# Kernel tuning notes

Measured on AMD Instinct MI355X. Metric: run time of the kernel, lower is better.

The kernel has to match this reference:

```python
import jax, jax.numpy as jnp
import numpy as np

B, L, D_IN = 16, 2048, 512
HID, H = 512, 8
D = HID // H          # head dim
FACTOR = 5
U = min(FACTOR * int(np.ceil(np.log(L))), L)  # u_q == u_k == 40 (L == S)


def setup_inputs() -> dict:
    key = jax.random.key(0)
    ks = jax.random.split(key, 8)
    s = 1.0 / np.sqrt(D_IN).astype(np.float32)
    return {
        "q_in": jax.random.normal(ks[0], (B, L, D_IN), jnp.float32),
        "k_in": jax.random.normal(ks[1], (B, L, D_IN), jnp.float32),
        "v_in": jax.random.normal(ks[2], (B, L, D_IN), jnp.float32),
        "Wq": jax.random.normal(ks[3], (D_IN, HID), jnp.float32) * s,
        "Wk": jax.random.normal(ks[4], (D_IN, HID), jnp.float32) * s,
        "Wv": jax.random.normal(ks[5], (D_IN, HID), jnp.float32) * s,
        "Wo": jax.random.normal(ks[6], (HID, HID // H), jnp.float32) / np.sqrt(HID).astype(np.float32),
        "indx_q_seq": jax.random.randint(ks[7], (L,), 0, L, dtype=jnp.int32),
    }


def reference(q_in, k_in, v_in, Wq, Wk, Wv, Wo, indx_q_seq):
    # projections + (memory-reinterpreting, as in the TF source) head reshape
    q = (q_in @ Wq).reshape(B, H, L, D)
    k = (k_in @ Wk).reshape(B, H, L, D)
    v = (v_in @ Wv).reshape(B, H, L, D)

    # --- _prob_qk ---
    # TF's chained gathers on the broadcast k_expand collapse to pairing
    # query s with the single key indx_q_seq[s]; all sample_k columns of
    # Q_K_sample are identical, so M = max - sum/L = dot * (1 - U/L).
    k_sel = k[:, :, indx_q_seq, :]                        # [B,H,L,D]
    dot = jnp.einsum('bhle,bhle->bhl', q, k_sel)          # [B,H,L]
    M = dot - dot * (jnp.float32(U) / jnp.float32(L))
    _, m_top = jax.lax.top_k(M, U)                        # [B,H,U]

    b_idx = jnp.arange(B)[:, None, None]
    h_idx = jnp.arange(H)[None, :, None]
    q_red = q[b_idx, h_idx, m_top]                        # [B,H,U,D]
    scores = jnp.einsum('bhue,bhle->bhul', q_red, k)      # [B,H,U,L]
    scores = scores * (1.0 / np.sqrt(D).astype(np.float32))

    # --- initial context: causal cumsum of values ---
    context = jnp.cumsum(v, axis=-2)                      # [B,H,L,D]

    # --- update context at the top-U query positions (causal mask) ---
    causal = jnp.arange(L)[None, None, None, :] > m_top[..., None]
    scores = jnp.where(causal, -jnp.inf, scores)
    attn = jax.nn.softmax(scores, axis=-1)                # [B,H,U,L]
    upd = jnp.einsum('bhul,bhld->bhud', attn, v)          # [B,H,U,D]
    context = context.at[b_idx, h_idx, m_top].set(upd)

    out = context.reshape(B, L, HID) @ Wo                 # [B,L,HID//H]
    return out
```

## Files before the change

kernel.cpp:

```cpp
#include <hip/hip_runtime.h>
#include <hip/hip_bf16.h>
#include <math.h>

#define B_   16
#define L_   2048
#define DIN  512
#define HID_ 512
#define H_   8
#define D_   64
#define U_   40
#define BH   (B_*H_)

typedef unsigned short u16;
typedef unsigned int u32;
typedef unsigned long long u64;
typedef __bf16 bf16x8 __attribute__((ext_vector_type(8)));
typedef float f32x4 __attribute__((ext_vector_type(4)));

__device__ __forceinline__ u16 f2bf(float x) {
  __bf16 b = (__bf16)x;
  return __builtin_bit_cast(unsigned short, b);
}
__device__ __forceinline__ float bf2f(u16 h) {
  return __uint_as_float(((unsigned)h) << 16);
}
__device__ __forceinline__ float bflo(u32 x) { return __uint_as_float(x << 16); }
__device__ __forceinline__ float bfhi(u32 x) { return __uint_as_float(x & 0xFFFF0000u); }
__device__ __forceinline__ u32 pk2(float a, float b) {
  return (u32)f2bf(a) | ((u32)f2bf(b) << 16);
}
__device__ __forceinline__ void gload16(const u16* g, u16* l) {
  __builtin_amdgcn_global_load_lds(
      (__attribute__((address_space(1))) void*)(g),
      (__attribute__((address_space(3))) void*)(l), 16, 0, 0);
}
__device__ __forceinline__ void gload16f(const float* g, float* l) {
  __builtin_amdgcn_global_load_lds(
      (__attribute__((address_space(1))) void*)(g),
      (__attribute__((address_space(3))) void*)(l), 16, 0, 0);
}
__device__ __forceinline__ u64 mkkey(float Mv, int l) {
  u32 fb = __float_as_uint(Mv);
  u32 mapped = (fb & 0x80000000u) ? ~fb : (fb | 0x80000000u);
  return ((u64)mapped << 32) | (u64)(0xFFFFFFFFu - (u32)l);
}

__global__ __launch_bounds__(256)
void wsplit3_kernel(const float* __restrict__ Wq, const float* __restrict__ Wk,
                    const float* __restrict__ Wv, u16* __restrict__ Bt3) {
  const float* W = (blockIdx.y == 0) ? Wq : (blockIdx.y == 1) ? Wk : Wv;
  u16* Bt = Bt3 + (size_t)blockIdx.y * 524288;
  int tid = blockIdx.x * 256 + threadIdx.x;
  int n = tid & 511, k = tid >> 9;
  float a = W[(size_t)k * 512 + n];
  u16 hi = f2bf(a);
  u16 lo = f2bf(a - bf2f(hi));
  int kb = k >> 5, kc = k & 31;
  int slotH = kc >> 3, wi = kc & 7;
  int swzH = (slotH     ^ (n & 7)) << 3;
  int swzL = ((4+slotH) ^ (n & 7)) << 3;
  Bt[(size_t)n * 1024 + kb * 64 + swzH + wi] = hi;
  Bt[(size_t)n * 1024 + kb * 64 + swzL + wi] = lo;
}

template<int NPASS, int OUTBF>
__global__ __launch_bounds__(256, 4)
void gemm_proj(const float* __restrict__ A, const u16* __restrict__ Bt,
               void* __restrict__ C) {
  __shared__ float Asf[128 * 32];
  __shared__ u16 Bs[128 * 64];
  const int bid = blockIdx.x;
  const int g = bid >> 3;
  const int xb = (bid & 7) + ((g >> 2) << 3);
  const int yb = g & 3;
  const int t = threadIdx.x;
  const int w = t >> 6, lane = t & 63;
  const int lhi = lane >> 4, l16 = lane & 15;
  const int row0 = xb * 128, col0 = yb * 128;
  const int wrow = (w >> 1) * 64, wcol = (w & 1) * 64;

  const u16* gB = Bt + (size_t)(col0 + w * 32 + (lane >> 3)) * 1024 + (lane & 7) * 8;
  u16* lB = &Bs[(w * 32) * 64];

  const int rA0 = w * 32 + (lane >> 3);
  const int swsl = lane & 7;

  f32x4 acc[4][4];
  #pragma unroll
  for (int i = 0; i < 4; ++i)
    #pragma unroll
    for (int j = 0; j < 4; ++j) acc[i][j] = (f32x4){0.f, 0.f, 0.f, 0.f};

  for (int kb = 0; kb < 16; ++kb) {
    #pragma unroll
    for (int i = 0; i < 4; ++i)
      gload16(gB + kb * 64 + (size_t)i * 8 * 1024, lB + i * 8 * 64);
    #pragma unroll
    for (int i = 0; i < 4; ++i) {
      int r = rA0 + i * 8;
      int slot = swsl ^ (r & 7);
      gload16f(A + (size_t)(row0 + r) * 512 + kb * 32 + slot * 4,
               &Asf[(w * 32 + i * 8) * 32]);
    }
    __syncthreads();

    bf16x8 bfH[4], bfL[4];
    #pragma unroll
    for (int j = 0; j < 4; ++j) {
      int cb = wcol + j * 16 + l16;
      bfH[j] = *reinterpret_cast<const bf16x8*>(
          &Bs[cb * 64 + ((lhi ^ (cb & 7)) << 3)]);
      if constexpr (NPASS == 3)
        bfL[j] = *reinterpret_cast<const bf16x8*>(
            &Bs[cb * 64 + (((4 + lhi) ^ (cb & 7)) << 3)]);
    }
    #pragma unroll
    for (int i = 0; i < 4; ++i) {
      int ra = wrow + i * 16 + l16;
      const f32x4 x0 = *reinterpret_cast<const f32x4*>(
          &Asf[ra * 32 + (((lhi * 2)       ^ (ra & 7)) << 2)]);
      const f32x4 x1 = *reinterpret_cast<const f32x4*>(
          &Asf[ra * 32 + ((((lhi * 2) + 1) ^ (ra & 7)) << 2)]);
      bf16x8 aH;
      aH[0] = (__bf16)x0[0]; aH[1] = (__bf16)x0[1];
      aH[2] = (__bf16)x0[2]; aH[3] = (__bf16)x0[3];
      aH[4] = (__bf16)x1[0]; aH[5] = (__bf16)x1[1];
      aH[6] = (__bf16)x1[2]; aH[7] = (__bf16)x1[3];
      #pragma unroll
      for (int j = 0; j < 4; ++j)
        acc[i][j] = __builtin_amdgcn_mfma_f32_16x16x32_bf16(aH, bfH[j], acc[i][j], 0, 0, 0);
      if constexpr (NPASS == 3) {
        bf16x8 aL;
        aL[0] = (__bf16)(x0[0] - (float)aH[0]); aL[1] = (__bf16)(x0[1] - (float)aH[1]);
        aL[2] = (__bf16)(x0[2] - (float)aH[2]); aL[3] = (__bf16)(x0[3] - (float)aH[3]);
        aL[4] = (__bf16)(x1[0] - (float)aH[4]); aL[5] = (__bf16)(x1[1] - (float)aH[5]);
        aL[6] = (__bf16)(x1[2] - (float)aH[6]); aL[7] = (__bf16)(x1[3] - (float)aH[7]);
        #pragma unroll
        for (int j = 0; j < 4; ++j)
          acc[i][j] = __builtin_amdgcn_mfma_f32_16x16x32_bf16(aH, bfL[j], acc[i][j], 0, 0, 0);
        #pragma unroll
        for (int j = 0; j < 4; ++j)
          acc[i][j] = __builtin_amdgcn_mfma_f32_16x16x32_bf16(aL, bfH[j], acc[i][j], 0, 0, 0);
      }
    }
    __syncthreads();
  }
  #pragma unroll
  for (int i = 0; i < 4; ++i)
    #pragma unroll
    for (int j = 0; j < 4; ++j)
      #pragma unroll
      for (int r = 0; r < 4; ++r) {
        size_t idx = (size_t)(row0 + wrow + i * 16 + lhi * 4 + r) * 512
                     + col0 + wcol + j * 16 + l16;
        if constexpr (OUTBF) ((u16*)C)[idx] = f2bf(acc[i][j][r]);
        else                 ((float*)C)[idx] = acc[i][j][r];
      }
}

__global__ __launch_bounds__(256)
void dotsel_kernel(const float* __restrict__ qp, const float* __restrict__ kp,
                   const int* __restrict__ indx, u64* __restrict__ cand) {
  __shared__ u64 keys[256];
  __shared__ u64 wmax[2][4];
  const int bh = blockIdx.x, ch = blockIdx.y;
  const int t = threadIdx.x, w = t >> 6, lane = t & 63;
  const size_t boff = (size_t)bh * 131072;
  const int l0 = ch * 256 + w * 64;
  const float cUL = 40.0f / 2048.0f;
  const int li = lane >> 4;
  const int dq = lane & 15;

  #pragma unroll 4
  for (int i = 0; i < 16; ++i) {
    int l = l0 + i * 4 + li;
    int ls = indx[l];
    float4 q4 = *reinterpret_cast<const float4*>(&qp[boff + (size_t)l * 64 + dq * 4]);
    float4 k4 = *reinterpret_cast<const float4*>(&kp[boff + (size_t)ls * 64 + dq * 4]);
    float p = q4.x * k4.x + q4.y * k4.y + q4.z * k4.z + q4.w * k4.w;
    p += __shfl_xor(p, 1, 64);
    p += __shfl_xor(p, 2, 64);
    p += __shfl_xor(p, 4, 64);
    p += __shfl_xor(p, 8, 64);
    if (dq == 0) {
      float Mv = p - p * cUL;
      keys[w * 64 + i * 4 + li] = mkkey(Mv, l);
    }
  }
  __syncthreads();

  u64 myk = keys[t];
  for (int u = 0; u < U_; ++u) {
    u64 b = myk;
    #pragma unroll
    for (int off = 32; off >= 1; off >>= 1) {
      u64 v = __shfl_xor(b, off, 64);
      if (v > b) b = v;
    }
    if (lane == 0) wmax[u & 1][w] = b;
    __syncthreads();
    const u64* wm = wmax[u & 1];
    u64 m = wm[0];
    if (wm[1] > m) m = wm[1];
    if (wm[2] > m) m = wm[2];
    if (wm[3] > m) m = wm[3];
    if (myk == m) myk = 0;
    if (t == 0) cand[((size_t)(bh * 8 + ch)) * U_ + u] = m;
  }
}

__global__ __launch_bounds__(64)
void merge_topk(const u64* __restrict__ cand, int* __restrict__ mtop) {
  const int bh = blockIdx.x;
  const int lane = threadIdx.x;
  u64 c0 = cand[(size_t)bh * 320 + 0 * 64 + lane];
  u64 c1 = cand[(size_t)bh * 320 + 1 * 64 + lane];
  u64 c2 = cand[(size_t)bh * 320 + 2 * 64 + lane];
  u64 c3 = cand[(size_t)bh * 320 + 3 * 64 + lane];
  u64 c4 = cand[(size_t)bh * 320 + 4 * 64 + lane];
  for (int u = 0; u < U_; ++u) {
    u64 b = c0;
    if (c1 > b) b = c1;
    if (c2 > b) b = c2;
    if (c3 > b) b = c3;
    if (c4 > b) b = c4;
    #pragma unroll
    for (int off = 32; off >= 1; off >>= 1) {
      u64 v = __shfl_xor(b, off, 64);
      if (v > b) b = v;
    }
    if (c0 == b) c0 = 0;
    if (c1 == b) c1 = 0;
    if (c2 == b) c2 = 0;
    if (c3 == b) c3 = 0;
    if (c4 == b) c4 = 0;
    if (lane == 0) mtop[bh * U_ + u] = (int)(0xFFFFFFFFu - (u32)b);
  }
}

__global__ __launch_bounds__(256)
void gather_q_kernel(const float* __restrict__ qp, const int* __restrict__ mtop,
                     u16* __restrict__ qredbf) {
  int tid = blockIdx.x * 256 + threadIdx.x;
  int s = tid >> 6;
  int d = tid & 63;
  int bh = s / 48;
  int u = s - bh * 48;
  float val = 0.f;
  if (u < U_) {
    int m = mtop[bh * U_ + u];
    val = qp[(size_t)bh * (L_ * D_) + (size_t)m * D_ + d] * 0.125f;
  }
  qredbf[tid] = f2bf(val);
}

__global__ __launch_bounds__(256)
void scores_mfma(const u16* __restrict__ qredbf, const float* __restrict__ kp,
                 const int* __restrict__ mtop, u16* __restrict__ S) {
  __shared__ u16 As[48 * 64];
  __shared__ u16 Bs[128 * 64];
  __shared__ int ms[U_];
  const int bh = blockIdx.x;
  const int l0 = blockIdx.y * 128;
  const int t = threadIdx.x, w = t >> 6, lane = t & 63;
  const int lhi = lane >> 4, l16 = lane & 15;

  for (int e = t; e < 384; e += 256) {
    int r = e >> 3, s = e & 7;
    *reinterpret_cast<uint4*>(&As[r * 64 + ((s ^ (r & 7)) << 3)]) =
        *reinterpret_cast<const uint4*>(&qredbf[(size_t)bh * 3072 + e * 8]);
  }
  #pragma unroll
  for (int ee = 0; ee < 4; ++ee) {
    int e = t + ee * 256;
    int r = e >> 3, s = e & 7;
    const float* src = &kp[(size_t)bh * 131072 + (size_t)(l0 + r) * 64 + s * 8];
    float4 va = *reinterpret_cast<const float4*>(src);
    float4 vb = *reinterpret_cast<const float4*>(src + 4);
    uint4 w4 = make_uint4(pk2(va.x, va.y), pk2(va.z, va.w),
                          pk2(vb.x, vb.y), pk2(vb.z, vb.w));
    *reinterpret_cast<uint4*>(&Bs[r * 64 + ((s ^ (r & 7)) << 3)]) = w4;
  }
  if (t < U_) ms[t] = mtop[bh * U_ + t];
  __syncthreads();

  f32x4 acc[3][2];
  #pragma unroll
  for (int m = 0; m < 3; ++m)
    #pragma unroll
    for (int n = 0; n < 2; ++n) acc[m][n] = (f32x4){0.f, 0.f, 0.f, 0.f};

  #pragma unroll
  for (int ks = 0; ks < 2; ++ks) {
    bf16x8 a[3], b[2];
    #pragma unroll
    for (int m = 0; m < 3; ++m) {
      int r = m * 16 + l16;
      a[m] = *reinterpret_cast<const bf16x8*>(
          &As[r * 64 + (((ks * 4 + lhi) ^ (r & 7)) << 3)]);
    }
    #pragma unroll
    for (int n = 0; n < 2; ++n) {
      int cb = w * 32 + n * 16 + l16;
      b[n] = *reinterpret_cast<const bf16x8*>(
          &Bs[cb * 64 + (((ks * 4 + lhi) ^ (cb & 7)) << 3)]);
    }
    #pragma unroll
    for (int m = 0; m < 3; ++m)
      #pragma unroll
      for (int n = 0; n < 2; ++n)
        acc[m][n] = __builtin_amdgcn_mfma_f32_16x16x32_bf16(a[m], b[n], acc[m][n], 0, 0, 0);
  }

  #pragma unroll
  for (int m = 0; m < 3; ++m)
    #pragma unroll
    for (int n = 0; n < 2; ++n)
      #pragma unroll
      for (int r = 0; r < 4; ++r) {
        int u = m * 16 + lhi * 4 + r;
        if (u < U_) {
          int l = l0 + w * 32 + n * 16 + l16;
          float val = acc[m][n][r];
          if (l > ms[u]) val = -INFINITY;
          S[((size_t)bh * 48 + u) * 2048 + l] = f2bf(val);
        }
      }
}

__global__ __launch_bounds__(256)
void softmax_kernel(u16* __restrict__ S) {
  __shared__ float red[4];
  const int rr = blockIdx.x;
  const int bh = rr / U_;
  const int u = rr - bh * U_;
  const int t = threadIdx.x;
  uint4* rp = reinterpret_cast<uint4*>(&S[((size_t)bh * 48 + u) * 2048]);
  uint4 raw = rp[t];
  float f[8];
  f[0] = bflo(raw.x); f[1] = bfhi(raw.x); f[2] = bflo(raw.y); f[3] = bfhi(raw.y);
  f[4] = bflo(raw.z); f[5] = bfhi(raw.z); f[6] = bflo(raw.w); f[7] = bfhi(raw.w);
  float m = f[0];
  #pragma unroll
  for (int i = 1; i < 8; ++i) m = fmaxf(m, f[i]);
  #pragma unroll
  for (int off = 32; off >= 1; off >>= 1) m = fmaxf(m, __shfl_xor(m, off, 64));
  if ((t & 63) == 0) red[t >> 6] = m;
  __syncthreads();
  m = fmaxf(fmaxf(red[0], red[1]), fmaxf(red[2], red[3]));
  __syncthreads();
  float s = 0.f;
  #pragma unroll
  for (int i = 0; i < 8; ++i) { f[i] = expf(f[i] - m); s += f[i]; }
  #pragma unroll
  for (int off = 32; off >= 1; off >>= 1) s += __shfl_xor(s, off, 64);
  if ((t & 63) == 0) red[t >> 6] = s;
  __syncthreads();
  s = red[0] + red[1] + red[2] + red[3];
  float inv = 1.0f / s;
  uint4 o;
  o.x = pk2(f[0] * inv, f[1] * inv);
  o.y = pk2(f[2] * inv, f[3] * inv);
  o.z = pk2(f[4] * inv, f[5] * inv);
  o.w = pk2(f[6] * inv, f[7] * inv);
  rp[t] = o;
}

__global__ __launch_bounds__(256)
void pv_mfma(const u16* __restrict__ Pbf, const u16* __restrict__ vbf,
             float* __restrict__ partial) {
  __shared__ u16 Ps[48 * 128];
  __shared__ u16 Vs[64 * 128];
  const int bh = blockIdx.x, kh = blockIdx.y;
  const int t = threadIdx.x, w = t >> 6, lane = t & 63;
  const int lhi = lane >> 4, l16 = lane & 15;
  const size_t vbase = (size_t)bh * 131072;
  f32x4 acc[3];
  #pragma unroll
  for (int m = 0; m < 3; ++m) acc[m] = (f32x4){0.f, 0.f, 0.f, 0.f};

  for (int ch = 0; ch < 2; ++ch) {
    const int lb = kh * 256 + ch * 128;
    for (int e = t; e < 768; e += 256) {
      int r = e >> 4, s = e & 15;
      int sw = (s & 8) | ((s & 7) ^ (r & 7));
      *reinterpret_cast<uint4*>(&Ps[r * 128 + (sw << 3)]) =
          *reinterpret_cast<const uint4*>(&Pbf[((size_t)bh * 48 + r) * 2048 + lb + s * 8]);
    }
    #pragma unroll
    for (int j = 0; j < 16; ++j) {
      int ll = w * 32 + 2 * j;
      u16 ua = vbf[vbase + (size_t)(lb + ll) * 64 + lane];
      u16 ub = vbf[vbase + (size_t)(lb + ll + 1) * 64 + lane];
      u32 pk = (u32)ua | ((u32)ub << 16);
      int s = ll >> 3;
      int sw = (s & 8) | ((s & 7) ^ (lane & 7));
      *reinterpret_cast<u32*>(&Vs[lane * 128 + (sw << 3) + (ll & 7)]) = pk;
    }
    __syncthreads();
    #pragma unroll
    for (int ks = 0; ks < 4; ++ks) {
      bf16x8 b;
      { int cb = w * 16 + l16; int s = ks * 4 + lhi;
        int sw = (s & 8) | ((s & 7) ^ (cb & 7));
        b = *reinterpret_cast<const bf16x8*>(&Vs[cb * 128 + (sw << 3)]); }
      #pragma unroll
      for (int m = 0; m < 3; ++m) {
        int r = m * 16 + l16; int s = ks * 4 + lhi;
        int sw = (s & 8) | ((s & 7) ^ (r & 7));
        bf16x8 a = *reinterpret_cast<const bf16x8*>(&Ps[r * 128 + (sw << 3)]);
        acc[m] = __builtin_amdgcn_mfma_f32_16x16x32_bf16(a, b, acc[m], 0, 0, 0);
      }
    }
    __syncthreads();
  }
  #pragma unroll
  for (int m = 0; m < 3; ++m)
    #pragma unroll
    for (int r = 0; r < 4; ++r) {
      int u = m * 16 + lhi * 4 + r;
      partial[(((size_t)kh * 128 + bh) * 48 + u) * 64 + w * 16 + l16] = acc[m][r];
    }
}

__global__ __launch_bounds__(256)
void cumsumA(const u16* __restrict__ vbf, float* __restrict__ seg32) {
  int bh = blockIdx.x, sg = blockIdx.y;
  int t = threadIdx.x, w = t >> 6, lane = t & 63;
  int g = sg * 4 + w;
  size_t base = (size_t)bh * 131072 + (size_t)g * 32 * 64;
  float s = 0.f;
  for (int i = 0; i < 32; ++i) s += bf2f(vbf[base + i * 64 + lane]);
  seg32[((size_t)bh * 64 + g) * 64 + lane] = s;
}
__global__ __launch_bounds__(256)
void cumsumB(const u16* __restrict__ vbf, const float* __restrict__ seg32,
             float* __restrict__ ctx) {
  int bh = blockIdx.x, sg = blockIdx.y;
  int t = threadIdx.x, w = t >> 6, lane = t & 63;
  int g = sg * 4 + w;
  float run = 0.f;
  for (int s = 0; s < g; ++s) run += seg32[((size_t)bh * 64 + s) * 64 + lane];
  size_t base = (size_t)bh * 131072 + (size_t)g * 32 * 64;
  for (int i = 0; i < 32; ++i) {
    run += bf2f(vbf[base + i * 64 + lane]);
    ctx[base + i * 64 + lane] = run;
  }
}

__global__ __launch_bounds__(256)
void scatter_kernel(const float* __restrict__ partial, const int* __restrict__ mtop,
                    float* __restrict__ ctx) {
  int tid = blockIdx.x * 256 + threadIdx.x;
  int s = tid >> 6;
  if (s >= BH * U_) return;
  int d = tid & 63;
  int bh = s / U_;
  int u = s - bh * U_;
  float a = 0.f;
  #pragma unroll
  for (int c = 0; c < 8; ++c)
    a += partial[(((size_t)(c * 128 + bh)) * 48 + u) * 64 + d];
  ctx[(size_t)bh * 131072 + (size_t)mtop[s] * 64 + d] = a;
}

__global__ __launch_bounds__(256)
void wo_prep(const float* __restrict__ Wo, u16* __restrict__ WoT) {
  int tid = blockIdx.x * 256 + threadIdx.x;
  int j = tid >> 9, k = tid & 511;
  float v = Wo[(size_t)k * 64 + j];
  int k0 = k & ~63, ko = k & 63;
  int ks = ko >> 5, kc = ko & 31;
  int slot = (ks * 4 + (kc >> 3)) ^ (j & 7);
  WoT[(size_t)j * 512 + k0 + (slot << 3) + (kc & 7)] = f2bf(v);
}

__global__ __launch_bounds__(256, 6)
void gemm_out(const float* __restrict__ ctx, const u16* __restrict__ WoT,
              float* __restrict__ out) {
  __shared__ u16 As[64 * 64];
  __shared__ u16 Bs[64 * 64];
  const int t = threadIdx.x, w = t >> 6, lane = t & 63;
  const int lhi = lane >> 4, l16 = lane & 15;
  const int row0 = blockIdx.x * 64;
  f32x4 acc[4];
  #pragma unroll
  for (int j = 0; j < 4; ++j) acc[j] = (f32x4){0.f, 0.f, 0.f, 0.f};

  for (int k0 = 0; k0 < 512; k0 += 64) {
    #pragma unroll
    for (int ii = 0; ii < 2; ++ii) {
      int e = t + ii * 256;
      int j = e >> 3, s = e & 7;
      gload16(WoT + (size_t)j * 512 + k0 + s * 8, Bs + (size_t)(w * 64 + ii * 256) * 8);
    }
    #pragma unroll
    for (int ii = 0; ii < 2; ++ii) {
      int e = t + ii * 256;
      int r = e >> 3, s = e & 7;
      const float* src = &ctx[(size_t)(row0 + r) * 512 + k0 + s * 8];
      float4 va = *reinterpret_cast<const float4*>(src);
      float4 vb = *reinterpret_cast<const float4*>(src + 4);
      uint4 w4 = make_uint4(pk2(va.x, va.y), pk2(va.z, va.w),
                            pk2(vb.x, vb.y), pk2(vb.z, vb.w));
      *reinterpret_cast<uint4*>(&As[r * 64 + ((s ^ (r & 7)) << 3)]) = w4;
    }
    __syncthreads();
    #pragma unroll
    for (int ks = 0; ks < 2; ++ks) {
      int r = w * 16 + l16;
      bf16x8 a = *reinterpret_cast<const bf16x8*>(
          &As[r * 64 + (((ks * 4 + lhi) ^ (r & 7)) << 3)]);
      #pragma unroll
      for (int jf = 0; jf < 4; ++jf) {
        int cb = jf * 16 + l16;
        bf16x8 b = *reinterpret_cast<const bf16x8*>(
            &Bs[cb * 64 + (((ks * 4 + lhi) ^ (cb & 7)) << 3)]);
        acc[jf] = __builtin_amdgcn_mfma_f32_16x16x32_bf16(a, b, acc[jf], 0, 0, 0);
      }
    }
    __syncthreads();
  }
  #pragma unroll
  for (int jf = 0; jf < 4; ++jf)
    #pragma unroll
    for (int r = 0; r < 4; ++r)
      out[(size_t)(row0 + w * 16 + lhi * 4 + r) * 64 + jf * 16 + l16] = acc[jf][r];
}

extern "C" void kernel_launch(void* const* d_in, const int* in_sizes, int n_in,
                              void* d_out, int out_size, void* d_ws, size_t ws_size,
                              hipStream_t stream) {
  const float* q_in = (const float*)d_in[0];
  const float* k_in = (const float*)d_in[1];
  const float* v_in = (const float*)d_in[2];
  const float* Wq   = (const float*)d_in[3];
  const float* Wk   = (const float*)d_in[4];
  const float* Wv   = (const float*)d_in[5];
  const float* Wo   = (const float*)d_in[6];
  const int*   indx = (const int*)d_in[7];
  float* out = (float*)d_out;

  float* ws = (float*)d_ws;
  float* qp   = ws;
  float* kp   = ws + 16777216;
  u16*   vbf  = (u16*)(ws + 33554432);
  u64*   cand = (u64*)(ws + 50331648);
  u16*   WoT  = (u16*)cand;
  u16*   qredbf = (u16*)(ws + 50593792);
  int*   mtop = (int*)(ws + 50921472);
  u16*   Bt3  = (u16*)d_out;
  u16*   S    = (u16*)qp;
  float* ctx  = qp;
  float* partial = kp;
  float* seg32   = kp + 3145728;

  const int M = B_ * L_;

  wsplit3_kernel<<<dim3(1024, 3), 256, 0, stream>>>(Wq, Wk, Wv, Bt3);

  gemm_proj<3, 0><<<1024, 256, 0, stream>>>(q_in, Bt3, qp);
  gemm_proj<3, 0><<<1024, 256, 0, stream>>>(k_in, Bt3 + 524288, kp);
  gemm_proj<1, 1><<<1024, 256, 0, stream>>>(v_in, Bt3 + 1048576, vbf);

  dotsel_kernel<<<dim3(BH, 8), 256, 0, stream>>>(qp, kp, indx, cand);
  merge_topk<<<BH, 64, 0, stream>>>(cand, mtop);
  gather_q_kernel<<<(BH * 48 * 64) / 256, 256, 0, stream>>>(qp, mtop, qredbf);

  scores_mfma<<<dim3(BH, 16), 256, 0, stream>>>(qredbf, kp, mtop, S);
  softmax_kernel<<<BH * U_, 256, 0, stream>>>(S);
  pv_mfma<<<dim3(BH, 8), 256, 0, stream>>>(S, vbf, partial);

  cumsumA<<<dim3(BH, 16), 256, 0, stream>>>(vbf, seg32);
  cumsumB<<<dim3(BH, 16), 256, 0, stream>>>(vbf, seg32, ctx);

  scatter_kernel<<<(BH * U_ * 64) / 256, 256, 0, stream>>>(partial, mtop, ctx);

  wo_prep<<<128, 256, 0, stream>>>(Wo, WoT);
  gemm_out<<<M / 64, 256, 0, stream>>>(ctx, WoT, out);
}
```

Measured before the change: 341.0 us.

## Fuse scores, softmax and PV into split-softmax kernel; bf16 context; double-buffer V GEMM

Replaces the separate scores, softmax and PV kernels with one fused kernel per 128-key chunk. It computes local max and sum, writes unnormalised partial PV results, and merges them in a small flash-style combine kernel, so the full score matrix never goes through global memory. The cumulative-sum context is stored in bf16 so the output GEMM can load it straight into LDS. The V projection GEMM gains double-buffered LDS staging. The trade-offs are more partial buffers (16 chunks instead of 8), extra rounding of the context, and lower occupancy in the V GEMM.

```diff
diff --git a/kernel.cpp b/kernel.cpp
--- a/kernel.cpp
+++ b/kernel.cpp
@@ -24,8 +24,6 @@
 __device__ __forceinline__ float bf2f(u16 h) {
   return __uint_as_float(((unsigned)h) << 16);
 }
-__device__ __forceinline__ float bflo(u32 x) { return __uint_as_float(x << 16); }
-__device__ __forceinline__ float bfhi(u32 x) { return __uint_as_float(x & 0xFFFF0000u); }
 __device__ __forceinline__ u32 pk2(float a, float b) {
   return (u32)f2bf(a) | ((u32)f2bf(b) << 16);
 }
@@ -63,10 +61,9 @@
   Bt[(size_t)n * 1024 + kb * 64 + swzL + wi] = lo;
 }
 
-template<int NPASS, int OUTBF>
 __global__ __launch_bounds__(256, 4)
-void gemm_proj(const float* __restrict__ A, const u16* __restrict__ Bt,
-               void* __restrict__ C) {
+void gemm_proj3(const float* __restrict__ A, const u16* __restrict__ Bt,
+                float* __restrict__ C) {
   __shared__ float Asf[128 * 32];
   __shared__ u16 Bs[128 * 64];
   const int bid = blockIdx.x;
@@ -81,7 +78,6 @@
 
   const u16* gB = Bt + (size_t)(col0 + w * 32 + (lane >> 3)) * 1024 + (lane & 7) * 8;
   u16* lB = &Bs[(w * 32) * 64];
-
   const int rA0 = w * 32 + (lane >> 3);
   const int swsl = lane & 7;
 
@@ -110,9 +106,8 @@
       int cb = wcol + j * 16 + l16;
       bfH[j] = *reinterpret_cast<const bf16x8*>(
           &Bs[cb * 64 + ((lhi ^ (cb & 7)) << 3)]);
-      if constexpr (NPASS == 3)
-        bfL[j] = *reinterpret_cast<const bf16x8*>(
-            &Bs[cb * 64 + (((4 + lhi) ^ (cb & 7)) << 3)]);
+      bfL[j] = *reinterpret_cast<const bf16x8*>(
+          &Bs[cb * 64 + (((4 + lhi) ^ (cb & 7)) << 3)]);
     }
     #pragma unroll
     for (int i = 0; i < 4; ++i) {
@@ -129,19 +124,17 @@
       #pragma unroll
       for (int j = 0; j < 4; ++j)
         acc[i][j] = __builtin_amdgcn_mfma_f32_16x16x32_bf16(aH, bfH[j], acc[i][j], 0, 0, 0);
-      if constexpr (NPASS == 3) {
-        bf16x8 aL;
-        aL[0] = (__bf16)(x0[0] - (float)aH[0]); aL[1] = (__bf16)(x0[1] - (float)aH[1]);
-        aL[2] = (__bf16)(x0[2] - (float)aH[2]); aL[3] = (__bf16)(x0[3] - (float)aH[3]);
-        aL[4] = (__bf16)(x1[0] - (float)aH[4]); aL[5] = (__bf16)(x1[1] - (float)aH[5]);
-        aL[6] = (__bf16)(x1[2] - (float)aH[6]); aL[7] = (__bf16)(x1[3] - (float)aH[7]);
-        #pragma unroll
-        for (int j = 0; j < 4; ++j)
-          acc[i][j] = __builtin_amdgcn_mfma_f32_16x16x32_bf16(aH, bfL[j], acc[i][j], 0, 0, 0);
-        #pragma unroll
-        for (int j = 0; j < 4; ++j)
-          acc[i][j] = __builtin_amdgcn_mfma_f32_16x16x32_bf16(aL, bfH[j], acc[i][j], 0, 0, 0);
-      }
+      bf16x8 aL;
+      aL[0] = (__bf16)(x0[0] - (float)aH[0]); aL[1] = (__bf16)(x0[1] - (float)aH[1]);
+      aL[2] = (__bf16)(x0[2] - (float)aH[2]); aL[3] = (__bf16)(x0[3] - (float)aH[3]);
+      aL[4] = (__bf16)(x1[0] - (float)aH[4]); aL[5] = (__bf16)(x1[1] - (float)aH[5]);
+      aL[6] = (__bf16)(x1[2] - (float)aH[6]); aL[7] = (__bf16)(x1[3] - (float)aH[7]);
+      #pragma unroll
+      for (int j = 0; j < 4; ++j)
+        acc[i][j] = __builtin_amdgcn_mfma_f32_16x16x32_bf16(aH, bfL[j], acc[i][j], 0, 0, 0);
+      #pragma unroll
+      for (int j = 0; j < 4; ++j)
+        acc[i][j] = __builtin_amdgcn_mfma_f32_16x16x32_bf16(aL, bfH[j], acc[i][j], 0, 0, 0);
     }
     __syncthreads();
   }
@@ -150,12 +143,86 @@
     #pragma unroll
     for (int j = 0; j < 4; ++j)
       #pragma unroll
-      for (int r = 0; r < 4; ++r) {
-        size_t idx = (size_t)(row0 + wrow + i * 16 + lhi * 4 + r) * 512
-                     + col0 + wcol + j * 16 + l16;
-        if constexpr (OUTBF) ((u16*)C)[idx] = f2bf(acc[i][j][r]);
-        else                 ((float*)C)[idx] = acc[i][j][r];
-      }
+      for (int r = 0; r < 4; ++r)
+        C[(size_t)(row0 + wrow + i * 16 + lhi * 4 + r) * 512
+          + col0 + wcol + j * 16 + l16] = acc[i][j][r];
+}
+
+__global__ __launch_bounds__(256, 2)
+void gemm_proj_v(const float* __restrict__ A, const u16* __restrict__ Bt,
+                 u16* __restrict__ C) {
+  __shared__ float Asf[2][128 * 32];
+  __shared__ u16 Bs[2][128 * 64];
+  const int bid = blockIdx.x;
+  const int g = bid >> 3;
+  const int xb = (bid & 7) + ((g >> 2) << 3);
+  const int yb = g & 3;
+  const int t = threadIdx.x;
+  const int w = t >> 6, lane = t & 63;
+  const int lhi = lane >> 4, l16 = lane & 15;
+  const int row0 = xb * 128, col0 = yb * 128;
+  const int wrow = (w >> 1) * 64, wcol = (w & 1) * 64;
+
+  const u16* gB = Bt + (size_t)(col0 + w * 32 + (lane >> 3)) * 1024 + (lane & 7) * 8;
+  const int rA0 = w * 32 + (lane >> 3);
+  const int swsl = lane & 7;
+
+  f32x4 acc[4][4];
+  #pragma unroll
+  for (int i = 0; i < 4; ++i)
+    #pragma unroll
+    for (int j = 0; j < 4; ++j) acc[i][j] = (f32x4){0.f, 0.f, 0.f, 0.f};
+
+#define STAGEV(KB, NB)                                                          \
+  { u16* lB = &Bs[NB][(w * 32) * 64];                                           \
+    _Pragma("unroll") for (int i = 0; i < 4; ++i)                               \
+      gload16(gB + (KB) * 64 + (size_t)i * 8 * 1024, lB + i * 8 * 64);          \
+    _Pragma("unroll") for (int i = 0; i < 4; ++i) {                             \
+      int r = rA0 + i * 8;                                                      \
+      int slot = swsl ^ (r & 7);                                                \
+      gload16f(A + (size_t)(row0 + r) * 512 + (KB) * 32 + slot * 4,             \
+               &Asf[NB][(w * 32 + i * 8) * 32]); } }
+
+  STAGEV(0, 0)
+  __syncthreads();
+
+  for (int kb = 0; kb < 16; ++kb) {
+    const int cur = kb & 1;
+    if (kb < 15) STAGEV(kb + 1, cur ^ 1)
+    bf16x8 bfH[4];
+    #pragma unroll
+    for (int j = 0; j < 4; ++j) {
+      int cb = wcol + j * 16 + l16;
+      bfH[j] = *reinterpret_cast<const bf16x8*>(
+          &Bs[cur][cb * 64 + ((lhi ^ (cb & 7)) << 3)]);
+    }
+    #pragma unroll
+    for (int i = 0; i < 4; ++i) {
+      int ra = wrow + i * 16 + l16;
+      const f32x4 x0 = *reinterpret_cast<const f32x4*>(
+          &Asf[cur][ra * 32 + (((lhi * 2)       ^ (ra & 7)) << 2)]);
+      const f32x4 x1 = *reinterpret_cast<const f32x4*>(
+          &Asf[cur][ra * 32 + ((((lhi * 2) + 1) ^ (ra & 7)) << 2)]);
+      bf16x8 aH;
+      aH[0] = (__bf16)x0[0]; aH[1] = (__bf16)x0[1];
+      aH[2] = (__bf16)x0[2]; aH[3] = (__bf16)x0[3];
+      aH[4] = (__bf16)x1[0]; aH[5] = (__bf16)x1[1];
+      aH[6] = (__bf16)x1[2]; aH[7] = (__bf16)x1[3];
+      #pragma unroll
+      for (int j = 0; j < 4; ++j)
+        acc[i][j] = __builtin_amdgcn_mfma_f32_16x16x32_bf16(aH, bfH[j], acc[i][j], 0, 0, 0);
+    }
+    __syncthreads();
+  }
+#undef STAGEV
+  #pragma unroll
+  for (int i = 0; i < 4; ++i)
+    #pragma unroll
+    for (int j = 0; j < 4; ++j)
+      #pragma unroll
+      for (int r = 0; r < 4; ++r)
+        C[(size_t)(row0 + wrow + i * 16 + lhi * 4 + r) * 512
+          + col0 + wcol + j * 16 + l16] = f2bf(acc[i][j][r]);
 }
 
 __global__ __launch_bounds__(256)
@@ -255,13 +322,17 @@
 }
 
 __global__ __launch_bounds__(256)
-void scores_mfma(const u16* __restrict__ qredbf, const float* __restrict__ kp,
-                 const int* __restrict__ mtop, u16* __restrict__ S) {
+void attn_fused(const u16* __restrict__ qredbf, const float* __restrict__ kp,
+                const u16* __restrict__ vbf, const int* __restrict__ mtop,
+                float* __restrict__ partial, float* __restrict__ msums) {
   __shared__ u16 As[48 * 64];
   __shared__ u16 Bs[128 * 64];
-  __shared__ int ms[U_];
-  const int bh = blockIdx.x;
-  const int l0 = blockIdx.y * 128;
+  __shared__ u16 Ps[48 * 128];
+  __shared__ int ms[48];
+  __shared__ float redm[4][48];
+  __shared__ float reds[4][48];
+  const int bh = blockIdx.x, chk = blockIdx.y;
+  const int l0 = chk * 128;
   const int t = threadIdx.x, w = t >> 6, lane = t & 63;
   const int lhi = lane >> 4, l16 = lane & 15;
 
@@ -281,7 +352,7 @@
                           pk2(vb.x, vb.y), pk2(vb.z, vb.w));
     *reinterpret_cast<uint4*>(&Bs[r * 64 + ((s ^ (r & 7)) << 3)]) = w4;
   }
-  if (t < U_) ms[t] = mtop[bh * U_ + t];
+  if (t < 48) ms[t] = (t < U_) ? mtop[bh * U_ + t] : -1;
   __syncthreads();
 
   f32x4 acc[3][2];
@@ -289,7 +360,6 @@
   for (int m = 0; m < 3; ++m)
     #pragma unroll
     for (int n = 0; n < 2; ++n) acc[m][n] = (f32x4){0.f, 0.f, 0.f, 0.f};
-
   #pragma unroll
   for (int ks = 0; ks < 2; ++ks) {
     bf16x8 a[3], b[2];
@@ -312,115 +382,137 @@
         acc[m][n] = __builtin_amdgcn_mfma_f32_16x16x32_bf16(a[m], b[n], acc[m][n], 0, 0, 0);
   }
 
-  #pragma unroll
-  for (int m = 0; m < 3; ++m)
-    #pragma unroll
-    for (int n = 0; n < 2; ++n)
-      #pragma unroll
-      for (int r = 0; r < 4; ++r) {
-        int u = m * 16 + lhi * 4 + r;
-        if (u < U_) {
-          int l = l0 + w * 32 + n * 16 + l16;
-          float val = acc[m][n][r];
-          if (l > ms[u]) val = -INFINITY;
-          S[((size_t)bh * 48 + u) * 2048 + l] = f2bf(val);
-        }
-      }
-}
-
-__global__ __launch_bounds__(256)
-void softmax_kernel(u16* __restrict__ S) {
-  __shared__ float red[4];
-  const int rr = blockIdx.x;
-  const int bh = rr / U_;
-  const int u = rr - bh * U_;
-  const int t = threadIdx.x;
-  uint4* rp = reinterpret_cast<uint4*>(&S[((size_t)bh * 48 + u) * 2048]);
-  uint4 raw = rp[t];
-  float f[8];
-  f[0] = bflo(raw.x); f[1] = bfhi(raw.x); f[2] = bflo(raw.y); f[3] = bfhi(raw.y);
-  f[4] = bflo(raw.z); f[5] = bfhi(raw.z); f[6] = bflo(raw.w); f[7] = bfhi(raw.w);
-  float m = f[0];
-  #pragma unroll
-  for (int i = 1; i < 8; ++i) m = fmaxf(m, f[i]);
-  #pragma unroll
-  for (int off = 32; off >= 1; off >>= 1) m = fmaxf(m, __shfl_xor(m, off, 64));
-  if ((t & 63) == 0) red[t >> 6] = m;
-  __syncthreads();
-  m = fmaxf(fmaxf(red[0], red[1]), fmaxf(red[2], red[3]));
-  __syncthreads();
-  float s = 0.f;
-  #pragma unroll
-  for (int i = 0; i < 8; ++i) { f[i] = expf(f[i] - m); s += f[i]; }
-  #pragma unroll
-  for (int off = 32; off >= 1; off >>= 1) s += __shfl_xor(s, off, 64);
-  if ((t & 63) == 0) red[t >> 6] = s;
-  __syncthreads();
-  s = red[0] + red[1] + red[2] + red[3];
-  float inv = 1.0f / s;
-  uint4 o;
-  o.x = pk2(f[0] * inv, f[1] * inv);
-  o.y = pk2(f[2] * inv, f[3] * inv);
-  o.z = pk2(f[4] * inv, f[5] * inv);
-  o.w = pk2(f[6] * inv, f[7] * inv);
-  rp[t] = o;
-}
-
-__global__ __launch_bounds__(256)
-void pv_mfma(const u16* __restrict__ Pbf, const u16* __restrict__ vbf,
-             float* __restrict__ partial) {
-  __shared__ u16 Ps[48 * 128];
-  __shared__ u16 Vs[64 * 128];
-  const int bh = blockIdx.x, kh = blockIdx.y;
-  const int t = threadIdx.x, w = t >> 6, lane = t & 63;
-  const int lhi = lane >> 4, l16 = lane & 15;
-  const size_t vbase = (size_t)bh * 131072;
-  f32x4 acc[3];
-  #pragma unroll
-  for (int m = 0; m < 3; ++m) acc[m] = (f32x4){0.f, 0.f, 0.f, 0.f};
-
-  for (int ch = 0; ch < 2; ++ch) {
-    const int lb = kh * 256 + ch * 128;
-    for (int e = t; e < 768; e += 256) {
-      int r = e >> 4, s = e & 15;
-      int sw = (s & 8) | ((s & 7) ^ (r & 7));
-      *reinterpret_cast<uint4*>(&Ps[r * 128 + (sw << 3)]) =
-          *reinterpret_cast<const uint4*>(&Pbf[((size_t)bh * 48 + r) * 2048 + lb + s * 8]);
-    }
-    #pragma unroll
-    for (int j = 0; j < 16; ++j) {
-      int ll = w * 32 + 2 * j;
-      u16 ua = vbf[vbase + (size_t)(lb + ll) * 64 + lane];
-      u16 ub = vbf[vbase + (size_t)(lb + ll + 1) * 64 + lane];
-      u32 pk = (u32)ua | ((u32)ub << 16);
-      int s = ll >> 3;
-      int sw = (s & 8) | ((s & 7) ^ (lane & 7));
-      *reinterpret_cast<u32*>(&Vs[lane * 128 + (sw << 3) + (ll & 7)]) = pk;
-    }
-    __syncthreads();
-    #pragma unroll
-    for (int ks = 0; ks < 4; ++ks) {
-      bf16x8 b;
-      { int cb = w * 16 + l16; int s = ks * 4 + lhi;
-        int sw = (s & 8) | ((s & 7) ^ (cb & 7));
-        b = *reinterpret_cast<const bf16x8*>(&Vs[cb * 128 + (sw << 3)]); }
-      #pragma unroll
-      for (int m = 0; m < 3; ++m) {
-        int r = m * 16 + l16; int s = ks * 4 + lhi;
-        int sw = (s & 8) | ((s & 7) ^ (r & 7));
-        bf16x8 a = *reinterpret_cast<const bf16x8*>(&Ps[r * 128 + (sw << 3)]);
-        acc[m] = __builtin_amdgcn_mfma_f32_16x16x32_bf16(a, b, acc[m], 0, 0, 0);
-      }
-    }
-    __syncthreads();
-  }
+  float val[3][2][4], mx[3][4];
   #pragma unroll
   for (int m = 0; m < 3; ++m)
     #pragma unroll
     for (int r = 0; r < 4; ++r) {
       int u = m * 16 + lhi * 4 + r;
-      partial[(((size_t)kh * 128 + bh) * 48 + u) * 64 + w * 16 + l16] = acc[m][r];
-    }
+      float v0 = acc[m][0][r], v1 = acc[m][1][r];
+      if (l0 + w * 32 + 0 * 16 + l16 > ms[u]) v0 = -INFINITY;
+      if (l0 + w * 32 + 1 * 16 + l16 > ms[u]) v1 = -INFINITY;
+      val[m][0][r] = v0; val[m][1][r] = v1;
+      mx[m][r] = fmaxf(v0, v1);
+    }
+  #pragma unroll
+  for (int off = 1; off <= 8; off <<= 1)
+    #pragma unroll
+    for (int m = 0; m < 3; ++m)
+      #pragma unroll
+      for (int r = 0; r < 4; ++r)
+        mx[m][r] = fmaxf(mx[m][r], __shfl_xor(mx[m][r], off, 64));
+  if (l16 == 0) {
+    #pragma unroll
+    for (int m = 0; m < 3; ++m)
+      #pragma unroll
+      for (int r = 0; r < 4; ++r)
+        redm[w][m * 16 + lhi * 4 + r] = mx[m][r];
+  }
+  __syncthreads();
+
+  float sx[3][4];
+  #pragma unroll
+  for (int m = 0; m < 3; ++m)
+    #pragma unroll
+    for (int r = 0; r < 4; ++r) {
+      int u = m * 16 + lhi * 4 + r;
+      float mv = fmaxf(fmaxf(redm[0][u], redm[1][u]), fmaxf(redm[2][u], redm[3][u]));
+      mv = (mv > -1e30f) ? mv : 0.f;
+      float p0 = __expf(val[m][0][r] - mv);
+      float p1 = __expf(val[m][1][r] - mv);
+      sx[m][r] = p0 + p1;
+      {
+        int l = w * 32 + 0 * 16 + l16, s = l >> 3;
+        int sw = (s & 8) | ((s & 7) ^ (u & 7));
+        Ps[u * 128 + (sw << 3) + (l & 7)] = f2bf(p0);
+      }
+      {
+        int l = w * 32 + 1 * 16 + l16, s = l >> 3;
+        int sw = (s & 8) | ((s & 7) ^ (u & 7));
+        Ps[u * 128 + (sw << 3) + (l & 7)] = f2bf(p1);
+      }
+    }
+  #pragma unroll
+  for (int off = 1; off <= 8; off <<= 1)
+    #pragma unroll
+    for (int m = 0; m < 3; ++m)
+      #pragma unroll
+      for (int r = 0; r < 4; ++r)
+        sx[m][r] += __shfl_xor(sx[m][r], off, 64);
+  if (l16 == 0) {
+    #pragma unroll
+    for (int m = 0; m < 3; ++m)
+      #pragma unroll
+      for (int r = 0; r < 4; ++r)
+        reds[w][m * 16 + lhi * 4 + r] = sx[m][r];
+  }
+  __syncthreads();
+
+  if (t < 48) {
+    float mv = fmaxf(fmaxf(redm[0][t], redm[1][t]), fmaxf(redm[2][t], redm[3][t]));
+    mv = (mv > -1e30f) ? mv : 0.f;
+    float sv = reds[0][t] + reds[1][t] + reds[2][t] + reds[3][t];
+    size_t o = (((size_t)chk * 128 + bh) * 48 + t) * 2;
+    msums[o] = mv; msums[o + 1] = sv;
+  }
+  const size_t vbase = (size_t)bh * 131072;
+  #pragma unroll
+  for (int j = 0; j < 16; ++j) {
+    int ll = w * 32 + 2 * j;
+    u16 ua = vbf[vbase + (size_t)(l0 + ll) * 64 + lane];
+    u16 ub = vbf[vbase + (size_t)(l0 + ll + 1) * 64 + lane];
+    u32 pk = (u32)ua | ((u32)ub << 16);
+    int s = ll >> 3;
+    int sw = (s & 8) | ((s & 7) ^ (lane & 7));
+    *reinterpret_cast<u32*>(&Bs[lane * 128 + (sw << 3) + (ll & 7)]) = pk;
+  }
+  __syncthreads();
+
+  f32x4 acc2[3];
+  #pragma unroll
+  for (int m = 0; m < 3; ++m) acc2[m] = (f32x4){0.f, 0.f, 0.f, 0.f};
+  #pragma unroll
+  for (int ks = 0; ks < 4; ++ks) {
+    bf16x8 b;
+    { int cb = w * 16 + l16; int s = ks * 4 + lhi;
+      int sw = (s & 8) | ((s & 7) ^ (cb & 7));
+      b = *reinterpret_cast<const bf16x8*>(&Bs[cb * 128 + (sw << 3)]); }
+    #pragma unroll
+    for (int m = 0; m < 3; ++m) {
+      int r = m * 16 + l16; int s = ks * 4 + lhi;
+      int sw = (s & 8) | ((s & 7) ^ (r & 7));
+      bf16x8 a = *reinterpret_cast<const bf16x8*>(&Ps[r * 128 + (sw << 3)]);
+      acc2[m] = __builtin_amdgcn_mfma_f32_16x16x32_bf16(a, b, acc2[m], 0, 0, 0);
+    }
+  }
+  #pragma unroll
+  for (int m = 0; m < 3; ++m)
+    #pragma unroll
+    for (int r = 0; r < 4; ++r) {
+      int u = m * 16 + lhi * 4 + r;
+      partial[(((size_t)chk * 128 + bh) * 48 + u) * 64 + w * 16 + l16] = acc2[m][r];
+    }
+}
+
+__global__ __launch_bounds__(256)
+void merge_pv(const float* __restrict__ partial, const float* __restrict__ msums,
+              float* __restrict__ upd) {
+  int tid = blockIdx.x * 256 + threadIdx.x;
+  int s = tid >> 6, d = tid & 63;
+  int bh = s / U_, u = s - bh * U_;
+  float mg = -INFINITY;
+  #pragma unroll
+  for (int c = 0; c < 16; ++c)
+    mg = fmaxf(mg, msums[(((size_t)c * 128 + bh) * 48 + u) * 2]);
+  float av = 0.f, sg = 0.f;
+  #pragma unroll
+  for (int c = 0; c < 16; ++c) {
+    size_t o = (((size_t)c * 128 + bh) * 48 + u) * 2;
+    float e = __expf(msums[o] - mg);
+    av += partial[(((size_t)c * 128 + bh) * 48 + u) * 64 + d] * e;
+    sg += msums[o + 1] * e;
+  }
+  upd[(size_t)s * 64 + d] = av / sg;
 }
 
 __global__ __launch_bounds__(256)
@@ -435,7 +527,7 @@
 }
 __global__ __launch_bounds__(256)
 void cumsumB(const u16* __restrict__ vbf, const float* __restrict__ seg32,
-             float* __restrict__ ctx) {
+             u16* __restrict__ ctxbf) {
   int bh = blockIdx.x, sg = blockIdx.y;
   int t = threadIdx.x, w = t >> 6, lane = t & 63;
   int g = sg * 4 + w;
@@ -444,24 +536,19 @@
   size_t base = (size_t)bh * 131072 + (size_t)g * 32 * 64;
   for (int i = 0; i < 32; ++i) {
     run += bf2f(vbf[base + i * 64 + lane]);
-    ctx[base + i * 64 + lane] = run;
-  }
-}
-
-__global__ __launch_bounds__(256)
-void scatter_kernel(const float* __restrict__ partial, const int* __restrict__ mtop,
-                    float* __restrict__ ctx) {
+    ctxbf[base + i * 64 + lane] = f2bf(run);
+  }
+}
+
+__global__ __launch_bounds__(256)
+void scatter_kernel(const float* __restrict__ upd, const int* __restrict__ mtop,
+                    u16* __restrict__ ctxbf) {
   int tid = blockIdx.x * 256 + threadIdx.x;
   int s = tid >> 6;
   if (s >= BH * U_) return;
   int d = tid & 63;
   int bh = s / U_;
-  int u = s - bh * U_;
-  float a = 0.f;
-  #pragma unroll
-  for (int c = 0; c < 8; ++c)
-    a += partial[(((size_t)(c * 128 + bh)) * 48 + u) * 64 + d];
-  ctx[(size_t)bh * 131072 + (size_t)mtop[s] * 64 + d] = a;
+  ctxbf[(size_t)bh * 131072 + (size_t)mtop[s] * 64 + d] = f2bf(upd[(size_t)s * 64 + d]);
 }
 
 __global__ __launch_bounds__(256)
@@ -476,7 +563,7 @@
 }
 
 __global__ __launch_bounds__(256, 6)
-void gemm_out(const float* __restrict__ ctx, const u16* __restrict__ WoT,
+void gemm_out(const u16* __restrict__ ctxbf, const u16* __restrict__ WoT,
               float* __restrict__ out) {
   __shared__ u16 As[64 * 64];
   __shared__ u16 Bs[64 * 64];
@@ -498,12 +585,8 @@
     for (int ii = 0; ii < 2; ++ii) {
       int e = t + ii * 256;
       int r = e >> 3, s = e & 7;
-      const float* src = &ctx[(size_t)(row0 + r) * 512 + k0 + s * 8];
-      float4 va = *reinterpret_cast<const float4*>(src);
-      float4 vb = *reinterpret_cast<const float4*>(src + 4);
-      uint4 w4 = make_uint4(pk2(va.x, va.y), pk2(va.z, va.w),
-                            pk2(vb.x, vb.y), pk2(vb.z, vb.w));
-      *reinterpret_cast<uint4*>(&As[r * 64 + ((s ^ (r & 7)) << 3)]) = w4;
+      gload16(ctxbf + (size_t)(row0 + r) * 512 + k0 + (s ^ (r & 7)) * 8,
+              As + (size_t)(w * 64 + ii * 256) * 8);
     }
     __syncthreads();
     #pragma unroll
@@ -550,32 +633,32 @@
   u16*   qredbf = (u16*)(ws + 50593792);
   int*   mtop = (int*)(ws + 50921472);
   u16*   Bt3  = (u16*)d_out;
-  u16*   S    = (u16*)qp;
-  float* ctx  = qp;
-  float* partial = kp;
-  float* seg32   = kp + 3145728;
+  float* partial = qp;
+  float* msums   = qp + 6291456;
+  float* upd     = qp + 6488064;
+  u16*   ctxbf = (u16*)kp;
+  float* seg32 = kp + 8388608;
 
   const int M = B_ * L_;
 
   wsplit3_kernel<<<dim3(1024, 3), 256, 0, stream>>>(Wq, Wk, Wv, Bt3);
 
-  gemm_proj<3, 0><<<1024, 256, 0, stream>>>(q_in, Bt3, qp);
-  gemm_proj<3, 0><<<1024, 256, 0, stream>>>(k_in, Bt3 + 524288, kp);
-  gemm_proj<1, 1><<<1024, 256, 0, stream>>>(v_in, Bt3 + 1048576, vbf);
+  gemm_proj3<<<1024, 256, 0, stream>>>(q_in, Bt3, qp);
+  gemm_proj3<<<1024, 256, 0, stream>>>(k_in, Bt3 + 524288, kp);
+  gemm_proj_v<<<1024, 256, 0, stream>>>(v_in, Bt3 + 1048576, vbf);
 
   dotsel_kernel<<<dim3(BH, 8), 256, 0, stream>>>(qp, kp, indx, cand);
   merge_topk<<<BH, 64, 0, stream>>>(cand, mtop);
   gather_q_kernel<<<(BH * 48 * 64) / 256, 256, 0, stream>>>(qp, mtop, qredbf);
 
-  scores_mfma<<<dim3(BH, 16), 256, 0, stream>>>(qredbf, kp, mtop, S);
-  softmax_kernel<<<BH * U_, 256, 0, stream>>>(S);
-  pv_mfma<<<dim3(BH, 8), 256, 0, stream>>>(S, vbf, partial);
+  attn_fused<<<dim3(BH, 16), 256, 0, stream>>>(qredbf, kp, vbf, mtop, partial, msums);
+  merge_pv<<<(BH * U_ * 64) / 256, 256, 0, stream>>>(partial, msums, upd);
 
   cumsumA<<<dim3(BH, 16), 256, 0, stream>>>(vbf, seg32);
-  cumsumB<<<dim3(BH, 16), 256, 0, stream>>>(vbf, seg32, ctx);
-
-  scatter_kernel<<<(BH * U_ * 64) / 256, 256, 0, stream>>>(partial, mtop, ctx);
+  cumsumB<<<dim3(BH, 16), 256, 0, stream>>>(vbf, seg32, ctxbf);
+
+  scatter_kernel<<<(BH * U_ * 64) / 256, 256, 0, stream>>>(upd, mtop, ctxbf);
 
   wo_prep<<<128, 256, 0, stream>>>(Wo, WoT);
-  gemm_out<<<M / 64, 256, 0, stream>>>(ctx, WoT, out);
-}
+  gemm_out<<<M / 64, 256, 0, stream>>>(ctxbf, WoT, out);
+}
```

Result: no change. 341.2 us (+0.0%).
